# Optimization experiments

Measured on AMD Instinct MI355X. Metric: run time of the kernel, lower is better.

The kernel has to match this reference:

```python
import jax, jax.numpy as jnp
import numpy as np

NUM_HEADS = 16
HEAD_DIM = 64  # model_dim // num_heads


def setup_inputs() -> dict:
    key = jax.random.key(0)
    ks = jax.random.split(key, 9)
    B, S, D = 2, 2048, 1024
    scale = 1.0 / np.sqrt(D)
    inp = {
        "tokens": jax.random.normal(ks[0], (B, S, D), dtype=jnp.float32),
        "Wq": jax.random.normal(ks[1], (D, D), dtype=jnp.float32) * scale,
        "bq": jnp.zeros((D,), dtype=jnp.float32),
        "Wk": jax.random.normal(ks[2], (D, D), dtype=jnp.float32) * scale,
        "bk": jnp.zeros((D,), dtype=jnp.float32),
        "Wv": jax.random.normal(ks[3], (D, D), dtype=jnp.float32) * scale,
        "bv": jnp.zeros((D,), dtype=jnp.float32),
        "Wo": jax.random.normal(ks[4], (D, D), dtype=jnp.float32) * scale,
        "bo": jnp.zeros((D,), dtype=jnp.float32),
    }
    return inp


def _split_heads(x):
    # [B, S, D] -> [B, H, S, d]
    B, S, D = x.shape
    return x.reshape(B, S, NUM_HEADS, HEAD_DIM).transpose(0, 2, 1, 3)


def reference(tokens, Wq, bq, Wk, bk, Wv, bv, Wo, bo):
    B, S, D = tokens.shape
    q = _split_heads(tokens @ Wq + bq)
    k = _split_heads(tokens @ Wk + bk)
    v = _split_heads(tokens @ Wv + bv)
    # shared logits: [B, H, S, S]
    logits = jnp.einsum("bhqd,bhkd->bhqk", q, k) / jnp.sqrt(
        jnp.asarray(HEAD_DIM, dtype=tokens.dtype))
    attn_neg = jax.nn.softmax(-logits, axis=-1)
    attn_pos = jax.nn.softmax(logits, axis=-1)
    feat_neg = jnp.einsum("bhqk,bhkd->bhqd", attn_neg, v)
    feat_pos = jnp.einsum("bhqk,bhkd->bhqd", attn_pos, v)
    # [B, H, S, d] -> [B, S, D]
    feat_neg = feat_neg.transpose(0, 2, 1, 3).reshape(B, S, D)
    feat_pos = feat_pos.transpose(0, 2, 1, 3).reshape(B, S, D)
    # shared output projection (proj[-1]) applied to both branches
    return (feat_neg @ Wo + bo, feat_pos @ Wo + bo)
```

## Files before the change

kernel.cpp:

```cpp
#include <hip/hip_runtime.h>
#include <hip/hip_bf16.h>

using bf16x8 = __attribute__((ext_vector_type(8))) short;
using f32x4  = __attribute__((ext_vector_type(4))) float;
using f32x16 = __attribute__((ext_vector_type(16))) float;
using u32x4  = __attribute__((ext_vector_type(4))) unsigned;

static constexpr int B_ = 2, S_ = 2048, D_ = 1024, H_ = 16, HD_ = 64;
static constexpr int BS_ = B_ * S_;
static constexpr float CP_ = 0.18033688011112042f;

__device__ __forceinline__ unsigned short bfbits(float x) {
    unsigned u = __builtin_bit_cast(unsigned, x);
    unsigned r = (u + 0x7fffu + ((u >> 16) & 1u)) >> 16;
    return (unsigned short)r;
}
__device__ __forceinline__ short bfs(float x) { return (short)bfbits(x); }

__device__ __forceinline__ unsigned cvt_pk_bf16(float lo, float hi) {
    unsigned r;
    asm("v_cvt_pk_bf16_f32 %0, %1, %2" : "=v"(r) : "v"(lo), "v"(hi));
    return r;
}
__device__ __forceinline__ void gload_lds16(const short* g, short* l) {
    __builtin_amdgcn_global_load_lds(
        (const __attribute__((address_space(1))) void*)g,
        (__attribute__((address_space(3))) void*)l, 16, 0, 0);
}

__global__ void cast_f32_bf16_kernel(const float* __restrict__ in,
                                     short* __restrict__ out, int n8) {
    int i = blockIdx.x * blockDim.x + threadIdx.x;
    if (i >= n8) return;
    const float4* p = (const float4*)in + (size_t)i * 2;
    float4 a = p[0], b = p[1];
    short tmp[8] = { bfs(a.x), bfs(a.y), bfs(a.z), bfs(a.w),
                     bfs(b.x), bfs(b.y), bfs(b.z), bfs(b.w) };
    *(int4*)(out + (size_t)i * 8) = *(int4*)tmp;
}

__global__ void transpose_cast4_kernel(const float* __restrict__ Wq,
                                       const float* __restrict__ Wk,
                                       const float* __restrict__ Wv,
                                       const float* __restrict__ Wo,
                                       short* __restrict__ WT) {
    __shared__ short tile[64][65];
    const float* srcs[4] = {Wq, Wk, Wv, Wo};
    const float* in = srcs[blockIdx.z];
    short* out = WT + (size_t)blockIdx.z * D_ * D_;
    int t = threadIdx.x;
    int r0 = blockIdx.y * 64, c0 = blockIdx.x * 64;
    int lr = t >> 2, lc0 = (t & 3) * 16;
    const float4* src = (const float4*)(in + (size_t)(r0 + lr) * D_ + c0 + lc0);
#pragma unroll
    for (int v = 0; v < 4; v++) {
        float4 f = src[v];
        tile[lr][lc0 + v * 4 + 0] = bfs(f.x);
        tile[lr][lc0 + v * 4 + 1] = bfs(f.y);
        tile[lr][lc0 + v * 4 + 2] = bfs(f.z);
        tile[lr][lc0 + v * 4 + 3] = bfs(f.w);
    }
    __syncthreads();
    int oc = t >> 2, os0 = (t & 3) * 16;
    short tmp[16];
#pragma unroll
    for (int j = 0; j < 16; j++) tmp[j] = tile[os0 + j][oc];
    short* dst = out + (size_t)(c0 + oc) * D_ + r0 + os0;
    *(int4*)(dst) = *(int4*)(tmp);
    *(int4*)(dst + 8) = *(int4*)(tmp + 8);
}

template <int MODE>
__global__ __launch_bounds__(256, 2)
void gemm_bt_kernel(const short* __restrict__ A, const short* __restrict__ BT,
                    const float* __restrict__ bp0, const float* __restrict__ bp1,
                    const float* __restrict__ bp2, void* __restrict__ Cout,
                    int M, int N, int K) {
    __shared__ __align__(16) short As[128 * 32];
    __shared__ __align__(16) short Bs[128 * 32];
    int t = threadIdx.x;
    int w = t >> 6, l = t & 63;
    int lq = l & 15, g = l >> 4;
    int rowBase = blockIdx.y * 128, colBase = blockIdx.x * 128;
    int wrow = (w >> 1) * 64, wcol = (w & 1) * 64;
    f32x4 acc[4][4] = {};
    const short* ap0 = A + (size_t)(rowBase + (t >> 2)) * K + (t & 3) * 8;
    const short* ap1 = ap0 + (size_t)64 * K;
    const short* bpA = BT + (size_t)(colBase + (t >> 2)) * K + (t & 3) * 8;
    const short* bpB = bpA + (size_t)64 * K;
    for (int kt = 0; kt < K; kt += 32) {
        __syncthreads();
        gload_lds16(ap0 + kt, &As[t * 8]);
        gload_lds16(ap1 + kt, &As[t * 8 + 2048]);
        gload_lds16(bpA + kt, &Bs[t * 8]);
        gload_lds16(bpB + kt, &Bs[t * 8 + 2048]);
        __syncthreads();
        bf16x8 af[4], bfr[4];
#pragma unroll
        for (int mi = 0; mi < 4; mi++)
            af[mi] = *(const bf16x8*)(&As[(wrow + mi * 16 + lq) * 32 + 8 * g]);
#pragma unroll
        for (int ni = 0; ni < 4; ni++)
            bfr[ni] = *(const bf16x8*)(&Bs[(wcol + ni * 16 + lq) * 32 + 8 * g]);
#pragma unroll
        for (int mi = 0; mi < 4; mi++)
#pragma unroll
            for (int ni = 0; ni < 4; ni++)
                acc[mi][ni] = __builtin_amdgcn_mfma_f32_16x16x32_bf16(
                    af[mi], bfr[ni], acc[mi][ni], 0, 0, 0);
    }
#pragma unroll
    for (int mi = 0; mi < 4; mi++)
#pragma unroll
        for (int ni = 0; ni < 4; ni++) {
            int col = colBase + wcol + ni * 16 + lq;
            float bias, scale = 1.0f;
            if (MODE == 0) {
                const float* bp = (col < 1024) ? bp0 : ((col < 2048) ? bp1 : bp2);
                bias = bp[col & 1023];
                if (col < 1024) scale = CP_;
            } else {
                bias = bp0[col];
            }
#pragma unroll
            for (int r = 0; r < 4; r++) {
                int row = rowBase + wrow + mi * 16 + 4 * g + r;
                float v = (acc[mi][ni][r] + bias) * scale;
                if (MODE == 1)
                    ((float*)Cout)[(size_t)row * N + col] = v;
                else
                    ((short*)Cout)[(size_t)row * N + col] = bfs(v);
            }
        }
}

__global__ void pack_qk_kernel(const short* __restrict__ QKV,
                               short* __restrict__ Qf, short* __restrict__ Kf) {
    int t = threadIdx.x;
    int l = t & 63, hf = t >> 6;
    int tile = blockIdx.x;
    int h = blockIdx.y;
    int z = blockIdx.z; int b = z & 1, src = z >> 1;
    int s = tile * 32 + (l & 31);
    int d = 16 * hf + 8 * (l >> 5);
    const short* sp = QKV + (size_t)(b * S_ + s) * 3072 + src * 1024 + h * 64 + d;
    short* dst = (src ? Kf : Qf) +
                 ((((size_t)(b * H_ + h) * 64 + tile) * 4 + hf) * 64 + l) * 8;
    *(int4*)dst = *(const int4*)sp;
}

__global__ void pack_v_kernel(const short* __restrict__ QKV,
                              short* __restrict__ Vf) {
    __shared__ short Vl[256][68];
    int t = threadIdx.x;
    int sgrp = blockIdx.x, h = blockIdx.y, b = blockIdx.z;
    const short* sp = QKV + (size_t)(b * S_ + sgrp * 256 + t) * 3072 + 2048 + h * 64;
#pragma unroll
    for (int c = 0; c < 8; c++)
        *(int4*)(&Vl[t][c * 8]) = *(const int4*)(sp + c * 8);
    __syncthreads();
    int l = t & 63, hf = (t >> 6) & 1, dblk = t >> 7;
    int h2 = l >> 5, d = dblk * 32 + (l & 31);
    short* dstbase = Vf + (size_t)(b * H_ + h) * 131072;
#pragma unroll
    for (int k = 0; k < 8; k++) {
        short tmp[8];
#pragma unroll
        for (int j = 0; j < 8; j++) {
            int sl = k * 32 + 16 * hf + (j & 3) + 8 * (j >> 2) + 4 * h2;
            tmp[j] = Vl[sl][d];
        }
        int tile = sgrp * 8 + k;
        short* dst = dstbase + ((((size_t)tile * 2 + dblk) * 2 + hf) * 64 + l) * 8;
        *(int4*)dst = *(int4*)tmp;
    }
}

__global__ __launch_bounds__(256, 2)
void attn_kernel(const short* __restrict__ Qf, const short* __restrict__ Kf,
                 const short* __restrict__ Vf, short* __restrict__ featNeg,
                 short* __restrict__ featPos) {
    int t = threadIdx.x;
    int w = t >> 6, l = t & 63;
    int l31 = l & 31, h2 = l >> 5;
    int qtile = blockIdx.x;
    int hh = blockIdx.y, b = blockIdx.z;
    int qb0 = qtile * 128 + w * 32;
    size_t hb = (size_t)(b * H_ + hh) * 131072;

    bf16x8 qa[4];
    const short* qp = Qf + hb + ((size_t)(qb0 >> 5) * 4 * 64 + l) * 8;
#pragma unroll
    for (int hf = 0; hf < 4; hf++)
        qa[hf] = *(const bf16x8*)(qp + hf * 512);

    f32x16 acc[2][2] = {};
    float lsum[2] = {0.f, 0.f};

    const short* kp0 = Kf + hb + l * 8;
    const short* vp0 = Vf + hb + l * 8;

    for (int tile = 0; tile < 64; tile++) {
        const short* kp = kp0 + (size_t)tile * 2048;
        const short* vp = vp0 + (size_t)tile * 2048;
        bf16x8 ka[4];
#pragma unroll
        for (int hf = 0; hf < 4; hf++)
            ka[hf] = *(const bf16x8*)(kp + hf * 512);
        bf16x8 vb[2][2];
#pragma unroll
        for (int dblk = 0; dblk < 2; dblk++)
#pragma unroll
            for (int hf = 0; hf < 2; hf++)
                vb[dblk][hf] = *(const bf16x8*)(vp + (dblk * 2 + hf) * 512);

        f32x16 st = {};
#pragma unroll
        for (int hf = 0; hf < 4; hf++)
            st = __builtin_amdgcn_mfma_f32_32x32x16_bf16(ka[hf], qa[hf], st, 0, 0, 0);

#pragma unroll
        for (int br = 0; br < 2; br++) {
            unsigned c[8];
            float s0 = 0.f, s1 = 0.f;
#pragma unroll
            for (int i = 0; i < 8; i++) {
                float plo = __builtin_amdgcn_exp2f(br ? st[2 * i] : -st[2 * i]);
                float phi = __builtin_amdgcn_exp2f(br ? st[2 * i + 1] : -st[2 * i + 1]);
                if (i & 1) s1 += plo + phi; else s0 += plo + phi;
                c[i] = cvt_pk_bf16(plo, phi);
            }
            lsum[br] += s0 + s1;
            u32x4 lo4 = {c[0], c[1], c[2], c[3]};
            u32x4 hi4 = {c[4], c[5], c[6], c[7]};
            bf16x8 pa0 = __builtin_bit_cast(bf16x8, lo4);
            bf16x8 pa1 = __builtin_bit_cast(bf16x8, hi4);
#pragma unroll
            for (int dblk = 0; dblk < 2; dblk++) {
                acc[br][dblk] = __builtin_amdgcn_mfma_f32_32x32x16_bf16(
                    pa0, vb[dblk][0], acc[br][dblk], 0, 0, 0);
                acc[br][dblk] = __builtin_amdgcn_mfma_f32_32x32x16_bf16(
                    pa1, vb[dblk][1], acc[br][dblk], 0, 0, 0);
            }
        }
    }

#pragma unroll
    for (int br = 0; br < 2; br++) {
        float ls = lsum[br];
        ls += __shfl_xor(ls, 32);
        float inv = 1.0f / ls;
        short* dst = br ? featPos : featNeg;
#pragma unroll
        for (int r = 0; r < 16; r++) {
            int qr = (r & 3) + 8 * (r >> 2) + 4 * h2;
            float invq = __shfl(inv, qr);
            size_t row = (size_t)(b * S_ + qb0 + qr);
#pragma unroll
            for (int dblk = 0; dblk < 2; dblk++) {
                int col = hh * HD_ + dblk * 32 + l31;
                dst[row * D_ + col] = bfs(acc[br][dblk][r] * invq);
            }
        }
    }
}

extern "C" void kernel_launch(void* const* d_in, const int* in_sizes, int n_in,
                              void* d_out, int out_size, void* d_ws, size_t ws_size,
                              hipStream_t stream) {
    const float* tokens = (const float*)d_in[0];
    const float* Wq = (const float*)d_in[1];
    const float* bq = (const float*)d_in[2];
    const float* Wk = (const float*)d_in[3];
    const float* bk = (const float*)d_in[4];
    const float* Wv = (const float*)d_in[5];
    const float* bv = (const float*)d_in[6];
    const float* Wo = (const float*)d_in[7];
    const float* bo = (const float*)d_in[8];

    const size_t MB = 1048576;
    if (ws_size < 64 * MB) return;
    char* ws = (char*)d_ws;
    short* Xbf = (short*)(ws + 0 * MB);
    short* WT  = (short*)(ws + 8 * MB);
    short* QKV = (short*)(ws + 16 * MB);
    short* featNeg = (short*)(ws + 16 * MB);
    short* featPos = (short*)(ws + 24 * MB);
    short* Qf = (short*)(ws + 40 * MB);
    short* Kf = (short*)(ws + 48 * MB);
    short* Vf = (short*)(ws + 56 * MB);

    cast_f32_bf16_kernel<<<2048, 256, 0, stream>>>(tokens, Xbf, BS_ * D_ / 8);

    transpose_cast4_kernel<<<dim3(16, 16, 4), 256, 0, stream>>>(Wq, Wk, Wv, Wo, WT);

    gemm_bt_kernel<0><<<dim3(3072 / 128, BS_ / 128), 256, 0, stream>>>(
        Xbf, WT, bq, bk, bv, QKV, BS_, 3072, D_);

    pack_qk_kernel<<<dim3(64, 16, 4), 256, 0, stream>>>(QKV, Qf, Kf);
    pack_v_kernel<<<dim3(8, 16, 2), 256, 0, stream>>>(QKV, Vf);

    attn_kernel<<<dim3(S_ / 128, H_, B_), 256, 0, stream>>>(Qf, Kf, Vf, featNeg, featPos);

    gemm_bt_kernel<1><<<dim3(D_ / 128, 2 * BS_ / 128), 256, 0, stream>>>(
        featNeg, WT + (size_t)3 * D_ * D_, bo, nullptr, nullptr, d_out,
        2 * BS_, D_, D_);
}
```

Before: 230.3 us.

## Remap blocks per XCD, compute softmax row sums via MFMA, add setprio

Grids for the GEMMs and the attention kernel are flattened to 1D and remapped so consecutive logical tiles land on the same XCD (bid&7 striding). This is meant to improve L2 reuse of shared K/V and weight tiles. The attention kernel now computes the softmax denominators with extra MFMAs against a ones vector instead of VALU adds plus shuffles. It also raises wave priority around MFMA sections and unrolls the key loop by two. The ones-MFMA adds matrix work and accumulator registers, which may affect occupancy.

```diff
diff --git a/kernel.cpp b/kernel.cpp
--- a/kernel.cpp
+++ b/kernel.cpp
@@ -75,13 +75,16 @@
 void gemm_bt_kernel(const short* __restrict__ A, const short* __restrict__ BT,
                     const float* __restrict__ bp0, const float* __restrict__ bp1,
                     const float* __restrict__ bp2, void* __restrict__ Cout,
-                    int M, int N, int K) {
+                    int M, int N, int K, int nBx, int cpx) {
     __shared__ __align__(16) short As[128 * 32];
     __shared__ __align__(16) short Bs[128 * 32];
+    int bid = blockIdx.x;
+    int wg = (bid & 7) * cpx + (bid >> 3);
+    int bx = wg % nBx, by = wg / nBx;
     int t = threadIdx.x;
     int w = t >> 6, l = t & 63;
     int lq = l & 15, g = l >> 4;
-    int rowBase = blockIdx.y * 128, colBase = blockIdx.x * 128;
+    int rowBase = by * 128, colBase = bx * 128;
     int wrow = (w >> 1) * 64, wcol = (w & 1) * 64;
     f32x4 acc[4][4] = {};
     const short* ap0 = A + (size_t)(rowBase + (t >> 2)) * K + (t & 3) * 8;
@@ -180,11 +183,12 @@
 void attn_kernel(const short* __restrict__ Qf, const short* __restrict__ Kf,
                  const short* __restrict__ Vf, short* __restrict__ featNeg,
                  short* __restrict__ featPos) {
+    int bid = blockIdx.x;
+    int wg = (bid & 7) * 64 + (bid >> 3);
+    int qtile = wg & 15, hh = (wg >> 4) & 15, b = wg >> 8;
     int t = threadIdx.x;
     int w = t >> 6, l = t & 63;
     int l31 = l & 31, h2 = l >> 5;
-    int qtile = blockIdx.x;
-    int hh = blockIdx.y, b = blockIdx.z;
     int qb0 = qtile * 128 + w * 32;
     size_t hb = (size_t)(b * H_ + hh) * 131072;
 
@@ -194,12 +198,17 @@
     for (int hf = 0; hf < 4; hf++)
         qa[hf] = *(const bf16x8*)(qp + hf * 512);
 
+    bf16x8 ones;
+#pragma unroll
+    for (int j = 0; j < 8; j++) ones[j] = (short)0x3F80;
+
     f32x16 acc[2][2] = {};
-    float lsum[2] = {0.f, 0.f};
+    f32x16 acc_l[2] = {};
 
     const short* kp0 = Kf + hb + l * 8;
     const short* vp0 = Vf + hb + l * 8;
 
+#pragma unroll 2
     for (int tile = 0; tile < 64; tile++) {
         const short* kp = kp0 + (size_t)tile * 2048;
         const short* vp = vp0 + (size_t)tile * 2048;
@@ -215,26 +224,26 @@
                 vb[dblk][hf] = *(const bf16x8*)(vp + (dblk * 2 + hf) * 512);
 
         f32x16 st = {};
+        __builtin_amdgcn_s_setprio(1);
 #pragma unroll
         for (int hf = 0; hf < 4; hf++)
             st = __builtin_amdgcn_mfma_f32_32x32x16_bf16(ka[hf], qa[hf], st, 0, 0, 0);
+        __builtin_amdgcn_s_setprio(0);
 
 #pragma unroll
         for (int br = 0; br < 2; br++) {
             unsigned c[8];
-            float s0 = 0.f, s1 = 0.f;
 #pragma unroll
             for (int i = 0; i < 8; i++) {
                 float plo = __builtin_amdgcn_exp2f(br ? st[2 * i] : -st[2 * i]);
                 float phi = __builtin_amdgcn_exp2f(br ? st[2 * i + 1] : -st[2 * i + 1]);
-                if (i & 1) s1 += plo + phi; else s0 += plo + phi;
                 c[i] = cvt_pk_bf16(plo, phi);
             }
-            lsum[br] += s0 + s1;
             u32x4 lo4 = {c[0], c[1], c[2], c[3]};
             u32x4 hi4 = {c[4], c[5], c[6], c[7]};
             bf16x8 pa0 = __builtin_bit_cast(bf16x8, lo4);
             bf16x8 pa1 = __builtin_bit_cast(bf16x8, hi4);
+            __builtin_amdgcn_s_setprio(1);
 #pragma unroll
             for (int dblk = 0; dblk < 2; dblk++) {
                 acc[br][dblk] = __builtin_amdgcn_mfma_f32_32x32x16_bf16(
@@ -242,19 +251,19 @@
                 acc[br][dblk] = __builtin_amdgcn_mfma_f32_32x32x16_bf16(
                     pa1, vb[dblk][1], acc[br][dblk], 0, 0, 0);
             }
+            acc_l[br] = __builtin_amdgcn_mfma_f32_32x32x16_bf16(pa0, ones, acc_l[br], 0, 0, 0);
+            acc_l[br] = __builtin_amdgcn_mfma_f32_32x32x16_bf16(pa1, ones, acc_l[br], 0, 0, 0);
+            __builtin_amdgcn_s_setprio(0);
         }
     }
 
 #pragma unroll
     for (int br = 0; br < 2; br++) {
-        float ls = lsum[br];
-        ls += __shfl_xor(ls, 32);
-        float inv = 1.0f / ls;
         short* dst = br ? featPos : featNeg;
 #pragma unroll
         for (int r = 0; r < 16; r++) {
             int qr = (r & 3) + 8 * (r >> 2) + 4 * h2;
-            float invq = __shfl(inv, qr);
+            float invq = 1.0f / acc_l[br][r];
             size_t row = (size_t)(b * S_ + qb0 + qr);
 #pragma unroll
             for (int dblk = 0; dblk < 2; dblk++) {
@@ -294,15 +303,15 @@
 
     transpose_cast4_kernel<<<dim3(16, 16, 4), 256, 0, stream>>>(Wq, Wk, Wv, Wo, WT);
 
-    gemm_bt_kernel<0><<<dim3(3072 / 128, BS_ / 128), 256, 0, stream>>>(
-        Xbf, WT, bq, bk, bv, QKV, BS_, 3072, D_);
+    gemm_bt_kernel<0><<<768, 256, 0, stream>>>(
+        Xbf, WT, bq, bk, bv, QKV, BS_, 3072, D_, 24, 96);
 
     pack_qk_kernel<<<dim3(64, 16, 4), 256, 0, stream>>>(QKV, Qf, Kf);
     pack_v_kernel<<<dim3(8, 16, 2), 256, 0, stream>>>(QKV, Vf);
 
-    attn_kernel<<<dim3(S_ / 128, H_, B_), 256, 0, stream>>>(Qf, Kf, Vf, featNeg, featPos);
-
-    gemm_bt_kernel<1><<<dim3(D_ / 128, 2 * BS_ / 128), 256, 0, stream>>>(
+    attn_kernel<<<512, 256, 0, stream>>>(Qf, Kf, Vf, featNeg, featPos);
+
+    gemm_bt_kernel<1><<<512, 256, 0, stream>>>(
         featNeg, WT + (size_t)3 * D_ * D_, bo, nullptr, nullptr, d_out,
-        2 * BS_, D_, D_);
-}
+        2 * BS_, D_, D_, 8, 64);
+}
```

Measured after the change: 228.4 us. No clear change (-0.8%).
